# Kernel optimization log

Hardware: AMD Instinct MI355X
Metric: run time of the kernel (lower is better)

The kernel has to match this reference:

```python
import jax, jax.numpy as jnp
import numpy as np

LAMBDA_POS = 0.5
LAMBDA_RAD = 0.5
LAMBDA_UNPAIR = 0.5
EPS = 1e-6
N_PRED = 20


def setup_inputs() -> dict:
    key = jax.random.key(0)
    k1, k2 = jax.random.split(key)
    B, L = 1000000, 12
    pred = jax.random.uniform(k1, (B, N_PRED, 4), dtype=jnp.float32)
    label = jax.random.uniform(k2, (B, L, 4), dtype=jnp.float32)
    return {"pred": pred, "label": label}


def reference(pred, label):
    # pred: [B, 20, 4] (x, y, radius, prob); label: [B, L, 4]
    B, L = label.shape[0], label.shape[1]
    yl = label[:, :, None, :]   # [B, L, 1, 4]
    yp = pred[:, None, :, :]    # [B, 1, 20, 4]
    dist = jnp.sqrt((yl[..., 0] - yp[..., 0]) ** 2 + (yl[..., 1] - yp[..., 1]) ** 2)  # [B, L, 20]
    rdiff = jnp.abs(yl[..., 2] - yp[..., 2])  # [B, L, 20]
    cost = LAMBDA_POS * dist + LAMBDA_RAD * rdiff  # [B, L, 20]
    idx = jnp.argmin(cost, axis=-1)  # [B, L]

    matched = jnp.take_along_axis(pred, idx[:, :, None], axis=1)  # [B, L, 4]
    mdist = jnp.sqrt((label[..., 0] - matched[..., 0]) ** 2 + (label[..., 1] - matched[..., 1]) ** 2)
    mrdiff = jnp.abs(label[..., 2] - matched[..., 2])
    prob_pair = -jnp.log(matched[..., 3] + EPS)  # prob_loss(p, 1)
    loss_pair = jnp.sum(LAMBDA_POS * mdist + LAMBDA_RAD * mrdiff + prob_pair, axis=-1)  # [B]

    # pair_mask[i] = 1 if any label matched pred i
    mask = jnp.zeros((B, N_PRED), dtype=pred.dtype)
    mask = mask.at[jnp.arange(B)[:, None], idx].set(1.0)

    unpair_term = (-jnp.log(1.0 - pred[..., 3] + EPS) + LAMBDA_RAD * pred[..., 2]) * LAMBDA_UNPAIR  # [B, 20]
    loss_unpair = jnp.sum((1.0 - mask) * unpair_term, axis=-1)  # [B]

    return loss_pair / L + loss_unpair / (N_PRED - L)
```

## Files before the change

### kernel.cpp

```cpp
#include <hip/hip_runtime.h>
#include <math.h>

constexpr int NP = 20;
constexpr int NL = 12;

__device__ __forceinline__ float fast_log(float x) {
    return __builtin_amdgcn_logf(x) * 0.69314718055994530942f;
}

__global__ __launch_bounds__(256, 4) void myloss_kernel(
    const float4* __restrict__ pred,
    const float4* __restrict__ label,
    float* __restrict__ out,
    int B)
{
    int b = blockIdx.x * blockDim.x + threadIdx.x;
    if (b >= B) return;

    const float4* p4 = pred  + (size_t)b * NP;
    const float4* l4 = label + (size_t)b * NL;

    float px[NP], py[NP], pr[NP], pq[NP];
#pragma unroll
    for (int j = 0; j < NP; ++j) {
        float4 v = p4[j];
        px[j] = v.x; py[j] = v.y; pr[j] = v.z; pq[j] = v.w;
    }

    float lp = 0.0f;
    unsigned mask = 0u;

#pragma unroll 2
    for (int l = 0; l < NL; ++l) {
        float4 lv = l4[l];

        float m1[4], m2[4], mq[4];
        unsigned mb[4];
#pragma unroll
        for (int c = 0; c < 4; ++c) { m1[c] = INFINITY; m2[c] = INFINITY; mq[c] = 0.0f; mb[c] = 0u; }

#pragma unroll
        for (int i = 0; i < 5; ++i) {
#pragma unroll
            for (int c = 0; c < 4; ++c) {
                int p = c * 5 + i;
                float dx = lv.x - px[p];
                float dy = lv.y - py[p];
                float d2 = __builtin_fmaf(dy, dy, dx * dx);
                float dist = __builtin_amdgcn_sqrtf(d2);
                float s = dist + fabsf(lv.z - pr[p]);
                m2[c] = fminf(m2[c], fmaxf(m1[c], s));
                bool lt = s < m1[c];
                m1[c] = lt ? s : m1[c];
                mq[c] = lt ? pq[p] : mq[c];
                mb[c] = lt ? (1u << p) : mb[c];
            }
        }

        float g1 = m1[0], g2 = m2[0], qm = mq[0];
        unsigned bm = mb[0];
#pragma unroll
        for (int c = 1; c < 4; ++c) {
            g2 = fminf(fmaxf(g1, m1[c]), fminf(g2, m2[c]));
            bool sel = m1[c] < g1;
            g1 = sel ? m1[c] : g1;
            qm = sel ? mq[c] : qm;
            bm = sel ? mb[c] : bm;
        }

        if (g2 - g1 < 4e-6f) {
            float sm = INFINITY, qq = 0.0f;
            unsigned bb = 0u;
#pragma unroll 1
            for (int p = 0; p < NP; ++p) {
                float4 v = p4[p];
                float s;
                {
#pragma clang fp contract(off)
                    float dx = lv.x - v.x;
                    float dy = lv.y - v.y;
                    float d2 = dx * dx + dy * dy;
                    float dist = sqrtf(d2);
                    s = dist + fabsf(lv.z - v.z);
                }
                bool ltp = s < sm;
                sm = ltp ? s : sm;
                qq = ltp ? v.w : qq;
                bb = ltp ? (1u << p) : bb;
            }
            g1 = sm; qm = qq; bm = bb;
        }

        lp += 0.5f * g1 - fast_log(qm + 1e-6f);
        mask |= bm;
    }

    float lu = 0.0f;
#pragma unroll
    for (int p = 0; p < NP; ++p) {
        float t = (-fast_log(1.0f - pq[p] + 1e-6f) + 0.5f * pr[p]) * 0.5f;
        lu += (mask & (1u << p)) ? 0.0f : t;
    }

    out[b] = lp * (1.0f / 12.0f) + lu * 0.125f;
}

extern "C" void kernel_launch(void* const* d_in, const int* in_sizes, int n_in,
                              void* d_out, int out_size, void* d_ws, size_t ws_size,
                              hipStream_t stream) {
    const float4* pred  = (const float4*)d_in[0];
    const float4* label = (const float4*)d_in[1];
    float* out = (float*)d_out;
    int B = out_size;
    int threads = 256;
    int blocks = (B + threads - 1) / threads;
    hipLaunchKernelGGL(myloss_kernel, dim3(blocks), dim3(threads), 0, stream,
                       pred, label, out, B);
}
```

Before: 574.9 us.

## Invert loop order to stream preds over register-held labels

Result: slower. 600.6 us (+4.5%).

```diff
diff --git a/kernel.cpp b/kernel.cpp
--- a/kernel.cpp
+++ b/kernel.cpp
@@ -20,56 +20,52 @@
     const float4* p4 = pred  + (size_t)b * NP;
     const float4* l4 = label + (size_t)b * NL;
 
-    float px[NP], py[NP], pr[NP], pq[NP];
+    float lx[NL], ly[NL], lr[NL];
 #pragma unroll
-    for (int j = 0; j < NP; ++j) {
-        float4 v = p4[j];
-        px[j] = v.x; py[j] = v.y; pr[j] = v.z; pq[j] = v.w;
+    for (int l = 0; l < NL; ++l) {
+        float4 v = l4[l];
+        lx[l] = v.x; ly[l] = v.y; lr[l] = v.z;
     }
 
-    float lp = 0.0f;
-    unsigned mask = 0u;
+    float m1[NL], m2[NL], wq[NL], wr[NL];
+    unsigned wb[NL];
+#pragma unroll
+    for (int l = 0; l < NL; ++l) {
+        m1[l] = INFINITY; m2[l] = INFINITY;
+        wq[l] = 0.0f; wr[l] = 0.0f; wb[l] = 0u;
+    }
 
-#pragma unroll 2
-    for (int l = 0; l < NL; ++l) {
-        float4 lv = l4[l];
+    float lu_all = 0.0f;
 
-        float m1[4], m2[4], mq[4];
-        unsigned mb[4];
-#pragma unroll
-        for (int c = 0; c < 4; ++c) { m1[c] = INFINITY; m2[c] = INFINITY; mq[c] = 0.0f; mb[c] = 0u; }
+    float4 pv = p4[0];
+#pragma unroll 1
+    for (int p = 0; p < NP; ++p) {
+        float4 pnext = p4[(p < NP - 1) ? (p + 1) : (NP - 1)];
+        unsigned pbit = 1u << p;
+
+        lu_all += (-fast_log(1.0f - pv.w + 1e-6f) + 0.5f * pv.z) * 0.5f;
 
 #pragma unroll
-        for (int i = 0; i < 5; ++i) {
+        for (int l = 0; l < NL; ++l) {
+            float dx = lx[l] - pv.x;
+            float dy = ly[l] - pv.y;
+            float d2 = __builtin_fmaf(dy, dy, dx * dx);
+            float dist = __builtin_amdgcn_sqrtf(d2);
+            float s = dist + fabsf(lr[l] - pv.z);
+            m2[l] = fminf(m2[l], fmaxf(m1[l], s));
+            bool lt = s < m1[l];
+            m1[l] = lt ? s : m1[l];
+            wq[l] = lt ? pv.w : wq[l];
+            wr[l] = lt ? pv.z : wr[l];
+            wb[l] = lt ? pbit : wb[l];
+        }
+        pv = pnext;
+    }
+
 #pragma unroll
-            for (int c = 0; c < 4; ++c) {
-                int p = c * 5 + i;
-                float dx = lv.x - px[p];
-                float dy = lv.y - py[p];
-                float d2 = __builtin_fmaf(dy, dy, dx * dx);
-                float dist = __builtin_amdgcn_sqrtf(d2);
-                float s = dist + fabsf(lv.z - pr[p]);
-                m2[c] = fminf(m2[c], fmaxf(m1[c], s));
-                bool lt = s < m1[c];
-                m1[c] = lt ? s : m1[c];
-                mq[c] = lt ? pq[p] : mq[c];
-                mb[c] = lt ? (1u << p) : mb[c];
-            }
-        }
-
-        float g1 = m1[0], g2 = m2[0], qm = mq[0];
-        unsigned bm = mb[0];
-#pragma unroll
-        for (int c = 1; c < 4; ++c) {
-            g2 = fminf(fmaxf(g1, m1[c]), fminf(g2, m2[c]));
-            bool sel = m1[c] < g1;
-            g1 = sel ? m1[c] : g1;
-            qm = sel ? mq[c] : qm;
-            bm = sel ? mb[c] : bm;
-        }
-
-        if (g2 - g1 < 4e-6f) {
-            float sm = INFINITY, qq = 0.0f;
+    for (int l = 0; l < NL; ++l) {
+        if (m2[l] - m1[l] < 4e-6f) {
+            float sm = INFINITY, qq = 0.0f, rr = 0.0f;
             unsigned bb = 0u;
 #pragma unroll 1
             for (int p = 0; p < NP; ++p) {
@@ -77,32 +73,32 @@
                 float s;
                 {
 #pragma clang fp contract(off)
-                    float dx = lv.x - v.x;
-                    float dy = lv.y - v.y;
+                    float dx = lx[l] - v.x;
+                    float dy = ly[l] - v.y;
                     float d2 = dx * dx + dy * dy;
-                    float dist = sqrtf(d2);
-                    s = dist + fabsf(lv.z - v.z);
+                    s = sqrtf(d2) + fabsf(lr[l] - v.z);
                 }
                 bool ltp = s < sm;
                 sm = ltp ? s : sm;
                 qq = ltp ? v.w : qq;
+                rr = ltp ? v.z : rr;
                 bb = ltp ? (1u << p) : bb;
             }
-            g1 = sm; qm = qq; bm = bb;
+            m1[l] = sm; wq[l] = qq; wr[l] = rr; wb[l] = bb;
         }
-
-        lp += 0.5f * g1 - fast_log(qm + 1e-6f);
-        mask |= bm;
     }
 
-    float lu = 0.0f;
+    float lp = 0.0f;
+    unsigned seen = 0u;
 #pragma unroll
-    for (int p = 0; p < NP; ++p) {
-        float t = (-fast_log(1.0f - pq[p] + 1e-6f) + 0.5f * pr[p]) * 0.5f;
-        lu += (mask & (1u << p)) ? 0.0f : t;
+    for (int l = 0; l < NL; ++l) {
+        lp += 0.5f * m1[l] - fast_log(wq[l] + 1e-6f);
+        float t = (-fast_log(1.0f - wq[l] + 1e-6f) + 0.5f * wr[l]) * 0.5f;
+        lu_all -= (wb[l] & seen) ? 0.0f : t;
+        seen |= wb[l];
     }
 
-    out[b] = lp * (1.0f / 12.0f) + lu * 0.125f;
+    out[b] = lp * (1.0f / 12.0f) + lu_all * 0.125f;
 }
 
 extern "C" void kernel_launch(void* const* d_in, const int* in_sizes, int n_in,
```
